# Kernel optimization log

Hardware: AMD Instinct MI355X
Metric: run time of the kernel (lower is better)

## Reference

```python
import jax, jax.numpy as jnp
import numpy as np

N = 4096      # nodes in the propagation tree batch
D = 5000      # input (BoW/TF-IDF) feature dim
H = 512       # hidden_dim
C = 4         # n_class
L = 8         # number of tree levels


def setup_inputs() -> dict:
    key = jax.random.key(0)
    ks = jax.random.split(key, 12)
    init = lambda k, shape, fan: (jax.random.normal(k, shape, jnp.float32)
                                  / np.float32(np.sqrt(fan)))
    x = jax.random.normal(ks[0], (N, D), jnp.float32)
    adj = jax.random.uniform(ks[1], (N, N), jnp.float32)
    level = jax.random.randint(ks[2], (N,), 0, L, jnp.int32)
    return {
        "x": x,
        "adj": adj,
        "level": level,
        "E_w": init(ks[3], (H, D), D),
        "Wr": init(ks[4], (H, H), H),
        "Wz": init(ks[5], (H, H), H),
        "Ur": init(ks[6], (H, H), H),
        "Uz": init(ks[7], (H, H), H),
        "Wh": init(ks[8], (H, H), H),
        "Uh": init(ks[9], (H, H), H),
        "dec_w": init(ks[10], (C, H), H),
        "dec_b": jnp.zeros((C,), jnp.float32),
        "n_levels": L,
    }


def reference(x, adj, level, E_w, Wr, Wz, Ur, Uz, Wh, Uh, dec_w, dec_b, n_levels):
    # x_hat = E(x): [N, H]
    x_hat = x @ E_w.T
    # precompute gate input contributions from x_hat (constant across levels)
    xr = x_hat @ Wr.T
    xz = x_hat @ Wz.T
    xh = x_hat @ Wh.T
    h = jnp.zeros_like(x_hat)  # [N, H]
    # bottom-up over tree levels (deepest level first, root = level 0)
    for j in reversed(range(n_levels)):
        mask = (level == j).astype(x_hat.dtype)[:, None]  # [N, 1]
        # level_adj.mm(h): aggregate children states into current-level rows
        hs = mask * (adj @ h)                              # [N, H]
        r = jax.nn.sigmoid(xr + hs @ Ur.T)
        z = jax.nn.sigmoid(xz + hs @ Uz.T)
        hj_hat = jnp.tanh(xh + (hs * r) @ Uh.T)
        hj = (1.0 - z) * hs + z * hj_hat
        h = h + mask * hj
    # decoder(h): [N, C]
    return h @ dec_w.T + dec_b
```

## Files before the change

kernel.cpp:

```cpp
#include <hip/hip_runtime.h>
#include <math.h>


#define NNODE 4096
#define DD 5000
#define DP 5024
#define HH 512
#define HHHH 262144
#define LL 8
#define PMAX 640
#define AKS 8
#define AKC 512
#define STR 40
#define NHt 2097152
#define XCH 1696
#define EWP (HH * DP)

typedef __attribute__((ext_vector_type(8))) short short8v;
typedef __attribute__((ext_vector_type(4))) float float4v;

union fu { float f; unsigned u; };

__device__ __forceinline__ float sigf(float x) { return 1.0f / (1.0f + __expf(-x)); }
__device__ __forceinline__ float bf2f(ushort b) { fu v; v.u = ((unsigned)b) << 16; return v.f; }

__device__ __forceinline__ void splitpair(float a, float b, unsigned& hi,
                                          unsigned& mi, unsigned& lo) {
  const unsigned M = 0xFFFF0000u;
  fu A, B; A.f = a; B.f = b;
  hi = (A.u >> 16) | (B.u & M);
  fu Ah, Bh; Ah.u = A.u & M; Bh.u = B.u & M;
  float ra = a - Ah.f, rb = b - Bh.f;
  fu A1, B1; A1.f = ra; B1.f = rb;
  mi = (A1.u >> 16) | (B1.u & M);
  fu A1h, B1h; A1h.u = A1.u & M; B1h.u = B1.u & M;
  float ra2 = ra - A1h.f, rb2 = rb - B1h.f;
  fu A2, B2; A2.f = ra2; B2.f = rb2;
  lo = (A2.u >> 16) | (B2.u & M);
}

__device__ __forceinline__ void split8(const float* v, uint4& h, uint4& m, uint4& l) {
  splitpair(v[0], v[1], h.x, m.x, l.x);
  splitpair(v[2], v[3], h.y, m.y, l.y);
  splitpair(v[4], v[5], h.z, m.z, l.z);
  splitpair(v[6], v[7], h.w, m.w, l.w);
}

__device__ __forceinline__ void split1(float x, ushort& h, ushort& m, ushort& l) {
  const unsigned M = 0xFFFF0000u;
  fu a; a.f = x; h = (ushort)(a.u >> 16);
  fu ah; ah.u = a.u & M; float r = x - ah.f;
  fu b; b.f = r; m = (ushort)(b.u >> 16);
  fu bh; bh.u = b.u & M; float r2 = r - bh.f;
  fu c; c.f = r2; l = (ushort)(c.u >> 16);
}

template <int NB, int AROWS, int BROWS>
__device__ __forceinline__ void mfma6(const ushort* As, const ushort* Bs,
                                      int wm, int wn, int lr, int lg8,
                                      float4v (*acc)[NB]) {
  short8v a[2][3];
#pragma unroll
  for (int im = 0; im < 2; ++im)
#pragma unroll
    for (int p = 0; p < 3; ++p)
      a[im][p] = *reinterpret_cast<const short8v*>(
          &As[(p * AROWS + wm + 16 * im + lr) * STR + lg8]);
  short8v b[NB][3];
#pragma unroll
  for (int in = 0; in < NB; ++in)
#pragma unroll
    for (int p = 0; p < 3; ++p)
      b[in][p] = *reinterpret_cast<const short8v*>(
          &Bs[(p * BROWS + wn + 16 * in + lr) * STR + lg8]);
#pragma unroll
  for (int im = 0; im < 2; ++im)
#pragma unroll
    for (int in = 0; in < NB; ++in) {
      float4v c = acc[im][in];
      c = __builtin_amdgcn_mfma_f32_16x16x32_bf16(a[im][0], b[in][0], c, 0, 0, 0);
      c = __builtin_amdgcn_mfma_f32_16x16x32_bf16(a[im][0], b[in][1], c, 0, 0, 0);
      c = __builtin_amdgcn_mfma_f32_16x16x32_bf16(a[im][1], b[in][0], c, 0, 0, 0);
      c = __builtin_amdgcn_mfma_f32_16x16x32_bf16(a[im][0], b[in][2], c, 0, 0, 0);
      c = __builtin_amdgcn_mfma_f32_16x16x32_bf16(a[im][2], b[in][0], c, 0, 0, 0);
      c = __builtin_amdgcn_mfma_f32_16x16x32_bf16(a[im][1], b[in][1], c, 0, 0, 0);
      acc[im][in] = c;
    }
}

__global__ __launch_bounds__(256) void build_lists(const int* __restrict__ level,
                                                   int* __restrict__ counts,
                                                   int* __restrict__ rows, int N) {
  int i = blockIdx.x * blockDim.x + threadIdx.x;
  if (i < N) {
    int j = level[i];
    int p = atomicAdd(&counts[j], 1);
    rows[(size_t)j * N + p] = i;
  }
}

__global__ __launch_bounds__(256) void cast_all(
    const float* __restrict__ Ur, const float* __restrict__ Uz,
    const float* __restrict__ Uh, const float* __restrict__ Wr,
    const float* __restrict__ Wz, const float* __restrict__ Wh,
    ushort* __restrict__ urz3, ushort* __restrict__ uh3,
    ushort* __restrict__ w3s) {
  const int y = blockIdx.y;
  const float* src = (y == 0) ? Ur : (y == 1) ? Uz : (y == 2) ? Uh
                   : (y == 3) ? Wr : (y == 4) ? Wz : Wh;
  ushort* dst; size_t ps, off;
  if (y <= 1)      { dst = urz3; ps = 2 * (size_t)HHHH; off = (size_t)y * HHHH; }
  else if (y == 2) { dst = uh3;  ps = HHHH; off = 0; }
  else             { dst = w3s + (size_t)(y - 3) * 3 * HHHH; ps = HHHH; off = 0; }
  int i = (blockIdx.x * 256 + threadIdx.x) * 8;
  float4 t0 = *reinterpret_cast<const float4*>(src + i);
  float4 t1 = *reinterpret_cast<const float4*>(src + i + 4);
  float v[8] = {t0.x, t0.y, t0.z, t0.w, t1.x, t1.y, t1.z, t1.w};
  uint4 h, m, l;
  split8(v, h, m, l);
  *reinterpret_cast<uint4*>(dst + off + i) = h;
  *reinterpret_cast<uint4*>(dst + ps + off + i) = m;
  *reinterpret_cast<uint4*>(dst + 2 * ps + off + i) = l;
}

__global__ __launch_bounds__(256) void cast_ew(const float* __restrict__ Ew,
                                               ushort* __restrict__ ew3) {
  int idx = (blockIdx.x * 256 + threadIdx.x) * 8;
  int row = idx / DP, col = idx % DP;
  float v[8];
  if (col + 8 <= DD) {
    float4 t0 = *reinterpret_cast<const float4*>(Ew + (size_t)row * DD + col);
    float4 t1 = *reinterpret_cast<const float4*>(Ew + (size_t)row * DD + col + 4);
    v[0]=t0.x; v[1]=t0.y; v[2]=t0.z; v[3]=t0.w;
    v[4]=t1.x; v[5]=t1.y; v[6]=t1.z; v[7]=t1.w;
  } else {
#pragma unroll
    for (int i = 0; i < 8; ++i)
      v[i] = (col + i < DD) ? Ew[(size_t)row * DD + col + i] : 0.0f;
  }
  uint4 h, m, l;
  split8(v, h, m, l);
  *reinterpret_cast<uint4*>(ew3 + idx) = h;
  *reinterpret_cast<uint4*>(ew3 + EWP + idx) = m;
  *reinterpret_cast<uint4*>(ew3 + 2 * (size_t)EWP + idx) = l;
}

__global__ __launch_bounds__(256) void gemm_xhat_sk(const float* __restrict__ x,
                                                    const ushort* __restrict__ ew3,
                                                    float* __restrict__ xpart) {
  __shared__ ushort As[3 * 64 * STR];
  __shared__ ushort Bs[3 * 128 * STR];
  const int z = blockIdx.z;
  const int kb = z * XCH;
  const int kePad = min(kb + XCH, DP);
  const int keReal = min(kePad, DD);
  const int tid = threadIdx.x;
  const int bm = blockIdx.x * 64, bn = blockIdx.y * 128;
  const int wid = tid >> 6, lane = tid & 63;
  const int lr = lane & 15, lg = lane >> 4, lg8 = lg * 8;
  const int wm = (wid >> 1) * 32, wn = (wid & 1) * 64;
  const int ar = tid >> 2, akq = (tid & 3) * 8;
  const int br = tid >> 1, bkq = (tid & 1) * 16;
  const float* ap = x + (size_t)(bm + ar) * DD + kb + akq;
  const ushort* bph = ew3 + (size_t)(bn + br) * DP + kb + bkq;
  float4v acc[2][4];
#pragma unroll
  for (int i = 0; i < 2; ++i)
#pragma unroll
    for (int j = 0; j < 4; ++j) acc[i][j] = (float4v){0.f, 0.f, 0.f, 0.f};
  uint4 ah, am, al;
  short8v b0[3], b1[3];
  auto loadA = [&](int k0) {
    float v[8];
    if (k0 + 32 <= keReal) {
      float4 t0 = *reinterpret_cast<const float4*>(ap);
      float4 t1 = *reinterpret_cast<const float4*>(ap + 4);
      v[0]=t0.x; v[1]=t0.y; v[2]=t0.z; v[3]=t0.w;
      v[4]=t1.x; v[5]=t1.y; v[6]=t1.z; v[7]=t1.w;
    } else {
#pragma unroll
      for (int i = 0; i < 8; ++i) v[i] = (k0 + akq + i < keReal) ? ap[i] : 0.0f;
    }
    split8(v, ah, am, al);
    ap += 32;
  };
  auto loadB = [&]() {
#pragma unroll
    for (int p = 0; p < 3; ++p) {
      b0[p] = *reinterpret_cast<const short8v*>(bph + (size_t)p * EWP);
      b1[p] = *reinterpret_cast<const short8v*>(bph + (size_t)p * EWP + 8);
    }
    bph += 32;
  };
  loadA(kb); loadB();
  for (int k0 = kb; k0 < kePad; k0 += 32) {
    __syncthreads();
    *reinterpret_cast<uint4*>(&As[(0 * 64 + ar) * STR + akq]) = ah;
    *reinterpret_cast<uint4*>(&As[(1 * 64 + ar) * STR + akq]) = am;
    *reinterpret_cast<uint4*>(&As[(2 * 64 + ar) * STR + akq]) = al;
#pragma unroll
    for (int p = 0; p < 3; ++p) {
      *reinterpret_cast<short8v*>(&Bs[(p * 128 + br) * STR + bkq]) = b0[p];
      *reinterpret_cast<short8v*>(&Bs[(p * 128 + br) * STR + bkq + 8]) = b1[p];
    }
    __syncthreads();
    if (k0 + 32 < kePad) { loadA(k0 + 32); loadB(); }
    mfma6<4, 64, 128>(As, Bs, wm, wn, lr, lg8, acc);
  }
  float* C = xpart + (size_t)z * NHt;
#pragma unroll
  for (int im = 0; im < 2; ++im)
#pragma unroll
    for (int in = 0; in < 4; ++in)
#pragma unroll
      for (int r = 0; r < 4; ++r)
        C[(size_t)(bm + wm + im * 16 + lg * 4 + r) * HH + bn + wn + in * 16 + lr] =
            acc[im][in][r];
}

__global__ __launch_bounds__(256) void combine3(const float* __restrict__ p,
                                                ushort* __restrict__ xh3) {
  int i = (blockIdx.x * 256 + threadIdx.x) * 8;
  float v[8];
#pragma unroll
  for (int e = 0; e < 8; e += 4) {
    float4 a = *reinterpret_cast<const float4*>(p + i + e);
    float4 b = *reinterpret_cast<const float4*>(p + NHt + i + e);
    float4 c = *reinterpret_cast<const float4*>(p + 2 * (size_t)NHt + i + e);
    v[e + 0] = a.x + b.x + c.x; v[e + 1] = a.y + b.y + c.y;
    v[e + 2] = a.z + b.z + c.z; v[e + 3] = a.w + b.w + c.w;
  }
  uint4 h, m, l;
  split8(v, h, m, l);
  *reinterpret_cast<uint4*>(xh3 + i) = h;
  *reinterpret_cast<uint4*>(xh3 + NHt + i) = m;
  *reinterpret_cast<uint4*>(xh3 + 2 * (size_t)NHt + i) = l;
}

__global__ __launch_bounds__(256) void gemm_w36(const ushort* __restrict__ xh3,
                                                const ushort* __restrict__ w3s,
                                                float* __restrict__ xrzh) {
  const int z = blockIdx.z;
  const ushort* B = w3s + (size_t)z * 3 * HHHH;
  float* C = xrzh + (size_t)z * NHt;
  __shared__ ushort As[3 * 64 * STR];
  __shared__ ushort Bs[3 * 128 * STR];
  const int tid = threadIdx.x;
  const int bm = blockIdx.x * 64, bn = blockIdx.y * 128;
  const int wid = tid >> 6, lane = tid & 63;
  const int lr = lane & 15, lg = lane >> 4, lg8 = lg * 8;
  const int wm = (wid >> 1) * 32, wn = (wid & 1) * 64;
  const int ar = tid >> 2, akq = (tid & 3) * 8;
  const int br = tid >> 1, bkq = (tid & 1) * 16;
  const ushort* aph = xh3 + (size_t)(bm + ar) * HH + akq;
  const ushort* bph = B + (size_t)(bn + br) * HH + bkq;
  float4v acc[2][4];
#pragma unroll
  for (int i = 0; i < 2; ++i)
#pragma unroll
    for (int j = 0; j < 4; ++j) acc[i][j] = (float4v){0.f, 0.f, 0.f, 0.f};
  short8v a3[3], b0[3], b1[3];
  auto loadAll = [&]() {
#pragma unroll
    for (int p = 0; p < 3; ++p) {
      a3[p] = *reinterpret_cast<const short8v*>(aph + (size_t)p * NHt);
      b0[p] = *reinterpret_cast<const short8v*>(bph + (size_t)p * HHHH);
      b1[p] = *reinterpret_cast<const short8v*>(bph + (size_t)p * HHHH + 8);
    }
    aph += 32; bph += 32;
  };
  loadAll();
  for (int k0 = 0; k0 < HH; k0 += 32) {
    __syncthreads();
#pragma unroll
    for (int p = 0; p < 3; ++p) {
      *reinterpret_cast<short8v*>(&As[(p * 64 + ar) * STR + akq]) = a3[p];
      *reinterpret_cast<short8v*>(&Bs[(p * 128 + br) * STR + bkq]) = b0[p];
      *reinterpret_cast<short8v*>(&Bs[(p * 128 + br) * STR + bkq + 8]) = b1[p];
    }
    __syncthreads();
    if (k0 + 32 < HH) loadAll();
    mfma6<4, 64, 128>(As, Bs, wm, wn, lr, lg8, acc);
  }
#pragma unroll
  for (int im = 0; im < 2; ++im)
#pragma unroll
    for (int in = 0; in < 4; ++in)
#pragma unroll
      for (int r = 0; r < 4; ++r)
        C[(size_t)(bm + wm + im * 16 + lg * 4 + r) * HH + bn + wn + in * 16 + lr] =
            acc[im][in][r];
}

__global__ __launch_bounds__(256) void agg6(const float* __restrict__ adj,
                                            const ushort* __restrict__ hT3,
                                            const int* __restrict__ rows,
                                            const int* __restrict__ counts,
                                            int lvl, float* __restrict__ part) {
  const int cnt = min(counts[lvl], PMAX);
  const int bm = blockIdx.x * 32;
  if (bm >= cnt) return;
  const int* rl = rows + (size_t)lvl * NNODE;
  const int kb = blockIdx.z * AKC;
  const int bn = blockIdx.y * 128;
  __shared__ ushort As[3 * 32 * STR];
  __shared__ ushort Bs[3 * 128 * STR];
  const int tid = threadIdx.x;
  const int wid = tid >> 6, lane = tid & 63;
  const int lr = lane & 15, lg = lane >> 4, lg8 = lg * 8;
  const int wn = wid * 32;
  const int ar = (tid & 127) >> 2, akq = (tid & 3) * 8;
  const int br = tid >> 1, bkq = (tid & 1) * 16;
  int p0 = bm + ar;
  if (p0 >= cnt) p0 = cnt - 1;
  const float* ap = adj + (size_t)rl[p0] * NNODE + kb + akq;
  const ushort* bph = hT3 + (size_t)(bn + br) * NNODE + kb + bkq;
  float4v acc[2][2];
#pragma unroll
  for (int i = 0; i < 2; ++i)
#pragma unroll
    for (int j = 0; j < 2; ++j) acc[i][j] = (float4v){0.f, 0.f, 0.f, 0.f};
  uint4 ah, am, al;
  short8v b0[3], b1[3];
  auto loadA = [&]() {
    float4 t0 = *reinterpret_cast<const float4*>(ap);
    float4 t1 = *reinterpret_cast<const float4*>(ap + 4);
    float v[8] = {t0.x, t0.y, t0.z, t0.w, t1.x, t1.y, t1.z, t1.w};
    split8(v, ah, am, al);
    ap += 32;
  };
  auto loadB = [&]() {
#pragma unroll
    for (int p = 0; p < 3; ++p) {
      b0[p] = *reinterpret_cast<const short8v*>(bph + (size_t)p * NHt);
      b1[p] = *reinterpret_cast<const short8v*>(bph + (size_t)p * NHt + 8);
    }
    bph += 32;
  };
  if (tid < 128) loadA();
  loadB();
  for (int k0 = 0; k0 < AKC; k0 += 32) {
    __syncthreads();
    if (tid < 128) {
      *reinterpret_cast<uint4*>(&As[(0 * 32 + ar) * STR + akq]) = ah;
      *reinterpret_cast<uint4*>(&As[(1 * 32 + ar) * STR + akq]) = am;
      *reinterpret_cast<uint4*>(&As[(2 * 32 + ar) * STR + akq]) = al;
    }
#pragma unroll
    for (int p = 0; p < 3; ++p) {
      *reinterpret_cast<short8v*>(&Bs[(p * 128 + br) * STR + bkq]) = b0[p];
      *reinterpret_cast<short8v*>(&Bs[(p * 128 + br) * STR + bkq + 8]) = b1[p];
    }
    __syncthreads();
    if (k0 + 32 < AKC) {
      if (tid < 128) loadA();
      loadB();
    }
    mfma6<2, 32, 128>(As, Bs, 0, wn, lr, lg8, acc);
  }
  float* cp = part + (size_t)blockIdx.z * PMAX * HH;
#pragma unroll
  for (int im = 0; im < 2; ++im)
#pragma unroll
    for (int in = 0; in < 2; ++in)
#pragma unroll
      for (int r = 0; r < 4; ++r) {
        int p = bm + 16 * im + lg * 4 + r;
        if (p < cnt)
          cp[(size_t)p * HH + bn + wn + in * 16 + lr] = acc[im][in][r];
      }
}

__global__ __launch_bounds__(256) void agg_reduce6(const float* __restrict__ part,
                                                   float* __restrict__ hsf,
                                                   ushort* __restrict__ hs3) {
  int id = blockIdx.x * 256 + threadIdx.x;
  const int zs = PMAX * HH / 4;
  const float4* q = reinterpret_cast<const float4*>(part) + id;
  float4 s = q[0];
#pragma unroll
  for (int z = 1; z < AKS; ++z) {
    float4 t = q[(size_t)z * zs];
    s.x += t.x; s.y += t.y; s.z += t.z; s.w += t.w;
  }
  reinterpret_cast<float4*>(hsf)[id] = s;
  unsigned h0, m0, l0, h1, m1, l1;
  splitpair(s.x, s.y, h0, m0, l0);
  splitpair(s.z, s.w, h1, m1, l1);
  *reinterpret_cast<uint2*>(hs3 + (size_t)id * 4) = make_uint2(h0, h1);
  *reinterpret_cast<uint2*>(hs3 + PMAX * HH + (size_t)id * 4) = make_uint2(m0, m1);
  *reinterpret_cast<uint2*>(hs3 + 2 * PMAX * HH + (size_t)id * 4) = make_uint2(l0, l1);
}

__global__ __launch_bounds__(256) void gates_rz6(
    const ushort* __restrict__ hs3, const ushort* __restrict__ urz3,
    const float* __restrict__ xr, const float* __restrict__ xz,
    const float* __restrict__ hsf, const int* __restrict__ rows,
    const int* __restrict__ counts, int lvl, ushort* __restrict__ tb3,
    float* __restrict__ zb) {
  const int cnt = min(counts[lvl], PMAX);
  const int bm = blockIdx.x * 32;
  if (bm >= cnt) return;
  const int* rl = rows + (size_t)lvl * NNODE;
  const int bn = blockIdx.y * 64;
  __shared__ ushort As[3 * 32 * STR];
  __shared__ ushort Bs[3 * 64 * STR];
  const int tid = threadIdx.x;
  const int wid = tid >> 6, lane = tid & 63;
  const int lr = lane & 15, lg = lane >> 4, lg8 = lg * 8;
  const int wn = wid * 16;
  const int ar = (tid & 127) >> 2, akq = (tid & 3) * 8;
  const int br = tid >> 2, bkq = (tid & 3) * 8;
  const ushort* aph = hs3 + (size_t)(bm + ar) * HH + akq;
  const ushort* bph = urz3 + (size_t)(bn + br) * HH + bkq;
  float4v acc[2][1];
  acc[0][0] = (float4v){0.f, 0.f, 0.f, 0.f};
  acc[1][0] = (float4v){0.f, 0.f, 0.f, 0.f};
  short8v a3[3], b3[3];
  auto loadA = [&]() {
#pragma unroll
    for (int p = 0; p < 3; ++p)
      a3[p] = *reinterpret_cast<const short8v*>(aph + (size_t)p * PMAX * HH);
    aph += 32;
  };
  auto loadB = [&]() {
#pragma unroll
    for (int p = 0; p < 3; ++p)
      b3[p] = *reinterpret_cast<const short8v*>(bph + (size_t)p * 2 * HHHH);
    bph += 32;
  };
  if (tid < 128) loadA();
  loadB();
  for (int k0 = 0; k0 < HH; k0 += 32) {
    __syncthreads();
    if (tid < 128) {
#pragma unroll
      for (int p = 0; p < 3; ++p)
        *reinterpret_cast<short8v*>(&As[(p * 32 + ar) * STR + akq]) = a3[p];
    }
#pragma unroll
    for (int p = 0; p < 3; ++p)
      *reinterpret_cast<short8v*>(&Bs[(p * 64 + br) * STR + bkq]) = b3[p];
    __syncthreads();
    if (k0 + 32 < HH) {
      if (tid < 128) loadA();
      loadB();
    }
    mfma6<1, 32, 64>(As, Bs, 0, wn, lr, lg8, acc);
  }
  ushort* th = tb3;
  ushort* tm = tb3 + PMAX * HH;
  ushort* tl = tb3 + 2 * PMAX * HH;
#pragma unroll
  for (int im = 0; im < 2; ++im)
#pragma unroll
    for (int r = 0; r < 4; ++r) {
      int p = bm + 16 * im + lg * 4 + r;
      if (p < cnt) {
        int col = bn + wn + lr;
        int g = rl[p];
        if (col < HH) {
          float rr = sigf(xr[(size_t)g * HH + col] + acc[im][0][r]);
          float t = hsf[(size_t)p * HH + col] * rr;
          ushort h, m, l;
          split1(t, h, m, l);
          size_t idx = (size_t)p * HH + col;
          th[idx] = h; tm[idx] = m; tl[idx] = l;
        } else {
          int c = col - HH;
          zb[(size_t)p * HH + c] = sigf(xz[(size_t)g * HH + c] + acc[im][0][r]);
        }
      }
    }
}

__global__ __launch_bounds__(256) void gates_h6(
    const ushort* __restrict__ tb3, const ushort* __restrict__ uh3,
    const float* __restrict__ xh, const float* __restrict__ hsf,
    const float* __restrict__ zb, const int* __restrict__ rows,
    const int* __restrict__ counts, int lvl, ushort* __restrict__ hT3) {
  const int cnt = min(counts[lvl], PMAX);
  const int bm = blockIdx.x * 32;
  if (bm >= cnt) return;
  const int* rl = rows + (size_t)lvl * NNODE;
  const int bn = blockIdx.y * 64;
  __shared__ ushort As[3 * 32 * STR];
  __shared__ ushort Bs[3 * 64 * STR];
  const int tid = threadIdx.x;
  const int wid = tid >> 6, lane = tid & 63;
  const int lr = lane & 15, lg = lane >> 4, lg8 = lg * 8;
  const int wn = wid * 16;
  const int ar = (tid & 127) >> 2, akq = (tid & 3) * 8;
  const int br = tid >> 2, bkq = (tid & 3) * 8;
  const ushort* aph = tb3 + (size_t)(bm + ar) * HH + akq;
  const ushort* bph = uh3 + (size_t)(bn + br) * HH + bkq;
  float4v acc[2][1];
  acc[0][0] = (float4v){0.f, 0.f, 0.f, 0.f};
  acc[1][0] = (float4v){0.f, 0.f, 0.f, 0.f};
  short8v a3[3], b3[3];
  auto loadA = [&]() {
#pragma unroll
    for (int p = 0; p < 3; ++p)
      a3[p] = *reinterpret_cast<const short8v*>(aph + (size_t)p * PMAX * HH);
    aph += 32;
  };
  auto loadB = [&]() {
#pragma unroll
    for (int p = 0; p < 3; ++p)
      b3[p] = *reinterpret_cast<const short8v*>(bph + (size_t)p * HHHH);
    bph += 32;
  };
  if (tid < 128) loadA();
  loadB();
  for (int k0 = 0; k0 < HH; k0 += 32) {
    __syncthreads();
    if (tid < 128) {
#pragma unroll
      for (int p = 0; p < 3; ++p)
        *reinterpret_cast<short8v*>(&As[(p * 32 + ar) * STR + akq]) = a3[p];
    }
#pragma unroll
    for (int p = 0; p < 3; ++p)
      *reinterpret_cast<short8v*>(&Bs[(p * 64 + br) * STR + bkq]) = b3[p];
    __syncthreads();
    if (k0 + 32 < HH) {
      if (tid < 128) loadA();
      loadB();
    }
    mfma6<1, 32, 64>(As, Bs, 0, wn, lr, lg8, acc);
  }
  ushort* hp = hT3;
  ushort* mp = hT3 + NHt;
  ushort* lp = hT3 + 2 * (size_t)NHt;
#pragma unroll
  for (int im = 0; im < 2; ++im)
#pragma unroll
    for (int r = 0; r < 4; ++r) {
      int p = bm + 16 * im + lg * 4 + r;
      if (p < cnt) {
        int col = bn + wn + lr;
        int g = rl[p];
        size_t idx = (size_t)p * HH + col;
        float hh = tanhf(xh[(size_t)g * HH + col] + acc[im][0][r]);
        float zz = zb[idx];
        float hv = (1.0f - zz) * hsf[idx] + zz * hh;
        ushort h, m, l;
        split1(hv, h, m, l);
        size_t tix = (size_t)col * NNODE + g;
        hp[tix] = h; mp[tix] = m; lp[tix] = l;
      }
    }
}

__global__ __launch_bounds__(256) void lvl7_init(const float* __restrict__ xz,
                                                 const float* __restrict__ xh,
                                                 const int* __restrict__ rows,
                                                 const int* __restrict__ counts,
                                                 ushort* __restrict__ hT3) {
  const int cnt = min(counts[LL - 1], PMAX);
  int idx = blockIdx.x * 256 + threadIdx.x;
  int p = idx >> 6;
  int c0 = (idx & 63) * 8;
  if (p >= cnt) return;
  int g = rows[(size_t)(LL - 1) * NNODE + p];
  float4 z0 = *reinterpret_cast<const float4*>(xz + (size_t)g * HH + c0);
  float4 z1 = *reinterpret_cast<const float4*>(xz + (size_t)g * HH + c0 + 4);
  float4 h0 = *reinterpret_cast<const float4*>(xh + (size_t)g * HH + c0);
  float4 h1 = *reinterpret_cast<const float4*>(xh + (size_t)g * HH + c0 + 4);
  float zv[8] = {z0.x, z0.y, z0.z, z0.w, z1.x, z1.y, z1.z, z1.w};
  float hv[8] = {h0.x, h0.y, h0.z, h0.w, h1.x, h1.y, h1.z, h1.w};
#pragma unroll
  for (int i = 0; i < 8; ++i) {
    float val = sigf(zv[i]) * tanhf(hv[i]);
    ushort h, m, l;
    split1(val, h, m, l);
    size_t tix = (size_t)(c0 + i) * NNODE + g;
    hT3[tix] = h;
    hT3[NHt + tix] = m;
    hT3[2 * (size_t)NHt + tix] = l;
  }
}

__global__ __launch_bounds__(256) void decoder6(const ushort* __restrict__ hT3,
                                                const float* __restrict__ w,
                                                const float* __restrict__ b,
                                                float* __restrict__ out) {
  int g = blockIdx.x * 256 + threadIdx.x;
  float a0 = 0.f, a1 = 0.f, a2 = 0.f, a3 = 0.f;
#pragma unroll 4
  for (int c = 0; c < HH; ++c) {
    size_t idx = (size_t)c * NNODE + g;
    float hv = bf2f(hT3[idx]) + bf2f(hT3[NHt + idx]) +
               bf2f(hT3[2 * (size_t)NHt + idx]);
    a0 = fmaf(hv, w[c], a0);
    a1 = fmaf(hv, w[HH + c], a1);
    a2 = fmaf(hv, w[2 * HH + c], a2);
    a3 = fmaf(hv, w[3 * HH + c], a3);
  }
  float4 o = make_float4(a0 + b[0], a1 + b[1], a2 + b[2], a3 + b[3]);
  *reinterpret_cast<float4*>(out + (size_t)g * 4) = o;
}

extern "C" void kernel_launch(void* const* d_in, const int* in_sizes, int n_in,
                              void* d_out, int out_size, void* d_ws,
                              size_t ws_size, hipStream_t stream) {
  const float* x   = (const float*)d_in[0];
  const float* adj = (const float*)d_in[1];
  const int* level = (const int*)d_in[2];
  const float* E_w = (const float*)d_in[3];
  const float* Wr  = (const float*)d_in[4];
  const float* Wz  = (const float*)d_in[5];
  const float* Ur  = (const float*)d_in[6];
  const float* Uz  = (const float*)d_in[7];
  const float* Wh  = (const float*)d_in[8];
  const float* Uh  = (const float*)d_in[9];
  const float* dw  = (const float*)d_in[10];
  const float* db  = (const float*)d_in[11];

  char* wp = (char*)d_ws;
  ushort* urz3 = (ushort*)wp; wp += (size_t)3 * 2 * HHHH * 2;
  ushort* uh3  = (ushort*)wp; wp += (size_t)3 * HHHH * 2;
  ushort* w3s  = (ushort*)wp; wp += (size_t)3 * 3 * HHHH * 2;
  ushort* hT3  = (ushort*)wp; wp += (size_t)3 * NHt * 2;
  float*  xrzh = (float*)wp;  wp += (size_t)3 * NHt * 4;
  char* region = wp;
  ushort* ew3  = (ushort*)region;
  float*  part = (float*)region;
  ushort* tb3  = (ushort*)(region + (size_t)AKS * PMAX * HH * 4);
  float*  zb   = (float*)((char*)tb3 + (size_t)3 * PMAX * HH * 2);
  float*  hsf  = (float*)((char*)zb + (size_t)PMAX * HH * 4);
  ushort* hs3  = (ushort*)((char*)hsf + (size_t)PMAX * HH * 4);
  size_t regionBytes = (size_t)3 * EWP * 2;
  size_t lvlBytes = (size_t)AKS * PMAX * HH * 4 + (size_t)3 * PMAX * HH * 2 +
                    (size_t)PMAX * HH * 4 + (size_t)PMAX * HH * 4 +
                    (size_t)3 * PMAX * HH * 2;
  if (lvlBytes > regionBytes) regionBytes = lvlBytes;
  wp = region + regionBytes;
  int* counts = (int*)wp; wp += 64;
  int* rowsl  = (int*)wp; wp += (size_t)LL * NNODE * 4;
  if (ws_size < (size_t)(wp - (char*)d_ws)) return;

  ushort* xh3 = hT3;
  float* xpart = xrzh;

  hipMemsetAsync(counts, 0, 64, stream);
  build_lists<<<(NNODE + 255) / 256, 256, 0, stream>>>(level, counts, rowsl, NNODE);
  cast_all<<<dim3(HHHH / 8 / 256, 6), 256, 0, stream>>>(Ur, Uz, Uh, Wr, Wz, Wh,
                                                        urz3, uh3, w3s);
  cast_ew<<<dim3(HH * DP / 8 / 256), 256, 0, stream>>>(E_w, ew3);
  gemm_xhat_sk<<<dim3(NNODE / 64, HH / 128, 3), 256, 0, stream>>>(x, ew3, xpart);
  combine3<<<NHt / 8 / 256, 256, 0, stream>>>(xpart, xh3);
  gemm_w36<<<dim3(NNODE / 64, HH / 128, 3), 256, 0, stream>>>(xh3, w3s, xrzh);

  const float* xr  = xrzh;
  const float* xzp = xrzh + (size_t)NHt;
  const float* xhp = xrzh + (size_t)2 * NHt;

  hipMemsetAsync(hT3, 0, (size_t)3 * NHt * 2, stream);
  lvl7_init<<<PMAX * HH / 8 / 256, 256, 0, stream>>>(xzp, xhp, rowsl, counts, hT3);

  for (int j = LL - 2; j >= 0; --j) {
    agg6<<<dim3(PMAX / 32, HH / 128, AKS), 256, 0, stream>>>(adj, hT3, rowsl,
                                                             counts, j, part);
    agg_reduce6<<<PMAX * HH / 4 / 256, 256, 0, stream>>>(part, hsf, hs3);
    gates_rz6<<<dim3(PMAX / 32, 2 * HH / 64), 256, 0, stream>>>(
        hs3, urz3, xr, xzp, hsf, rowsl, counts, j, tb3, zb);
    gates_h6<<<dim3(PMAX / 32, HH / 64), 256, 0, stream>>>(
        tb3, uh3, xhp, hsf, zb, rowsl, counts, j, hT3);
  }
  decoder6<<<dim3(NNODE / 256), 256, 0, stream>>>(hT3, dw, db, (float*)d_out);
}
```

Baseline: 821.4 us.

## Store hidden states in level order and aggregate only over deeper-level nodes

Builds a level-ordered permutation of nodes, deepest levels first, and stores the transposed hidden states in that order. The aggregation GEMM for each level now runs its K loop only over nodes from deeper levels, since all other hidden rows are still zero. The split-K chunk size is computed dynamically. This removes roughly half of the multiply-accumulate work and the hidden-state reads in the adj @ h step. In exchange, adjacency values are now read as scattered per-element gathers through the permutation rather than contiguous vector loads, and the decoder and gate kernels must remap indices.

Measured after the change: 839.6 us. +2.2%, slower.

```diff
diff --git a/kernel.cpp b/kernel.cpp
--- a/kernel.cpp
+++ b/kernel.cpp
@@ -10,7 +10,6 @@
 #define LL 8
 #define PMAX 640
 #define AKS 8
-#define AKC 512
 #define STR 40
 #define NHt 2097152
 #define XCH 1696
@@ -23,6 +22,13 @@
 
 __device__ __forceinline__ float sigf(float x) { return 1.0f / (1.0f + __expf(-x)); }
 __device__ __forceinline__ float bf2f(ushort b) { fu v; v.u = ((unsigned)b) << 16; return v.f; }
+
+__device__ __forceinline__ int prefix_above(const int* __restrict__ counts,
+                                            int lvl) {
+  int s = 0;
+  for (int i = lvl + 1; i < LL; ++i) s += min(counts[i], PMAX);
+  return s;
+}
 
 __device__ __forceinline__ void splitpair(float a, float b, unsigned& hi,
                                           unsigned& mi, unsigned& lo) {
@@ -97,6 +103,16 @@
     int p = atomicAdd(&counts[j], 1);
     rows[(size_t)j * N + p] = i;
   }
+}
+
+__global__ __launch_bounds__(256) void build_order(const int* __restrict__ counts,
+                                                   const int* __restrict__ rows,
+                                                   int* __restrict__ actord) {
+  const int j = blockIdx.y;
+  const int cnt = min(counts[j], PMAX);
+  const int off = prefix_above(counts, j);
+  int p = blockIdx.x * 256 + threadIdx.x;
+  if (p < cnt) actord[off + p] = rows[(size_t)j * NNODE + p];
 }
 
 __global__ __launch_bounds__(256) void cast_all(
@@ -296,12 +312,16 @@
                                             const ushort* __restrict__ hT3,
                                             const int* __restrict__ rows,
                                             const int* __restrict__ counts,
+                                            const int* __restrict__ actord,
                                             int lvl, float* __restrict__ part) {
   const int cnt = min(counts[lvl], PMAX);
   const int bm = blockIdx.x * 32;
   if (bm >= cnt) return;
+  const int K = prefix_above(counts, lvl);
+  const int chunk = ((K + AKS * 32 - 1) / (AKS * 32)) * 32;
+  const int kb = blockIdx.z * chunk;
+  const int ke = min(kb + chunk, K);
   const int* rl = rows + (size_t)lvl * NNODE;
-  const int kb = blockIdx.z * AKC;
   const int bn = blockIdx.y * 128;
   __shared__ ushort As[3 * 32 * STR];
   __shared__ ushort Bs[3 * 128 * STR];
@@ -313,7 +333,8 @@
   const int br = tid >> 1, bkq = (tid & 1) * 16;
   int p0 = bm + ar;
   if (p0 >= cnt) p0 = cnt - 1;
-  const float* ap = adj + (size_t)rl[p0] * NNODE + kb + akq;
+  const float* adjrow = adj + (size_t)rl[p0] * NNODE;
+  const int* aop = actord + kb + akq;
   const ushort* bph = hT3 + (size_t)(bn + br) * NNODE + kb + bkq;
   float4v acc[2][2];
 #pragma unroll
@@ -323,11 +344,12 @@
   uint4 ah, am, al;
   short8v b0[3], b1[3];
   auto loadA = [&]() {
-    float4 t0 = *reinterpret_cast<const float4*>(ap);
-    float4 t1 = *reinterpret_cast<const float4*>(ap + 4);
-    float v[8] = {t0.x, t0.y, t0.z, t0.w, t1.x, t1.y, t1.z, t1.w};
+    int4 i0 = *reinterpret_cast<const int4*>(aop);
+    int4 i1 = *reinterpret_cast<const int4*>(aop + 4);
+    float v[8] = {adjrow[i0.x], adjrow[i0.y], adjrow[i0.z], adjrow[i0.w],
+                  adjrow[i1.x], adjrow[i1.y], adjrow[i1.z], adjrow[i1.w]};
     split8(v, ah, am, al);
-    ap += 32;
+    aop += 32;
   };
   auto loadB = [&]() {
 #pragma unroll
@@ -337,9 +359,11 @@
     }
     bph += 32;
   };
-  if (tid < 128) loadA();
-  loadB();
-  for (int k0 = 0; k0 < AKC; k0 += 32) {
+  if (kb < ke) {
+    if (tid < 128) loadA();
+    loadB();
+  }
+  for (int k0 = kb; k0 < ke; k0 += 32) {
     __syncthreads();
     if (tid < 128) {
       *reinterpret_cast<uint4*>(&As[(0 * 32 + ar) * STR + akq]) = ah;
@@ -352,7 +376,7 @@
       *reinterpret_cast<short8v*>(&Bs[(p * 128 + br) * STR + bkq + 8]) = b1[p];
     }
     __syncthreads();
-    if (k0 + 32 < AKC) {
+    if (k0 + 32 < ke) {
       if (tid < 128) loadA();
       loadB();
     }
@@ -482,6 +506,7 @@
   const int cnt = min(counts[lvl], PMAX);
   const int bm = blockIdx.x * 32;
   if (bm >= cnt) return;
+  const int poff = prefix_above(counts, lvl);
   const int* rl = rows + (size_t)lvl * NNODE;
   const int bn = blockIdx.y * 64;
   __shared__ ushort As[3 * 32 * STR];
@@ -546,7 +571,7 @@
         float hv = (1.0f - zz) * hsf[idx] + zz * hh;
         ushort h, m, l;
         split1(hv, h, m, l);
-        size_t tix = (size_t)col * NNODE + g;
+        size_t tix = (size_t)col * NNODE + (poff + p);
         hp[tix] = h; mp[tix] = m; lp[tix] = l;
       }
     }
@@ -574,7 +599,7 @@
     float val = sigf(zv[i]) * tanhf(hv[i]);
     ushort h, m, l;
     split1(val, h, m, l);
-    size_t tix = (size_t)(c0 + i) * NNODE + g;
+    size_t tix = (size_t)(c0 + i) * NNODE + p;
     hT3[tix] = h;
     hT3[NHt + tix] = m;
     hT3[2 * (size_t)NHt + tix] = l;
@@ -582,14 +607,16 @@
 }
 
 __global__ __launch_bounds__(256) void decoder6(const ushort* __restrict__ hT3,
+                                                const int* __restrict__ actord,
                                                 const float* __restrict__ w,
                                                 const float* __restrict__ b,
                                                 float* __restrict__ out) {
-  int g = blockIdx.x * 256 + threadIdx.x;
+  int p = blockIdx.x * 256 + threadIdx.x;
+  int g = actord[p];
   float a0 = 0.f, a1 = 0.f, a2 = 0.f, a3 = 0.f;
 #pragma unroll 4
   for (int c = 0; c < HH; ++c) {
-    size_t idx = (size_t)c * NNODE + g;
+    size_t idx = (size_t)c * NNODE + p;
     float hv = bf2f(hT3[idx]) + bf2f(hT3[NHt + idx]) +
                bf2f(hT3[2 * (size_t)NHt + idx]);
     a0 = fmaf(hv, w[c], a0);
@@ -638,6 +665,7 @@
   wp = region + regionBytes;
   int* counts = (int*)wp; wp += 64;
   int* rowsl  = (int*)wp; wp += (size_t)LL * NNODE * 4;
+  int* actord = (int*)wp; wp += (size_t)NNODE * 4;
   if (ws_size < (size_t)(wp - (char*)d_ws)) return;
 
   ushort* xh3 = hT3;
@@ -645,6 +673,8 @@
 
   hipMemsetAsync(counts, 0, 64, stream);
   build_lists<<<(NNODE + 255) / 256, 256, 0, stream>>>(level, counts, rowsl, NNODE);
+  build_order<<<dim3((PMAX + 255) / 256, LL), 256, 0, stream>>>(counts, rowsl,
+                                                                actord);
   cast_all<<<dim3(HHHH / 8 / 256, 6), 256, 0, stream>>>(Ur, Uz, Uh, Wr, Wz, Wh,
                                                         urz3, uh3, w3s);
   cast_ew<<<dim3(HH * DP / 8 / 256), 256, 0, stream>>>(E_w, ew3);
@@ -660,13 +690,14 @@
   lvl7_init<<<PMAX * HH / 8 / 256, 256, 0, stream>>>(xzp, xhp, rowsl, counts, hT3);
 
   for (int j = LL - 2; j >= 0; --j) {
-    agg6<<<dim3(PMAX / 32, HH / 128, AKS), 256, 0, stream>>>(adj, hT3, rowsl,
-                                                             counts, j, part);
+    agg6<<<dim3(PMAX / 32, HH / 128, AKS), 256, 0, stream>>>(
+        adj, hT3, rowsl, counts, actord, j, part);
     agg_reduce6<<<PMAX * HH / 4 / 256, 256, 0, stream>>>(part, hsf, hs3);
     gates_rz6<<<dim3(PMAX / 32, 2 * HH / 64), 256, 0, stream>>>(
         hs3, urz3, xr, xzp, hsf, rowsl, counts, j, tb3, zb);
     gates_h6<<<dim3(PMAX / 32, HH / 64), 256, 0, stream>>>(
         tb3, uh3, xhp, hsf, zb, rowsl, counts, j, hT3);
   }
-  decoder6<<<dim3(NNODE / 256), 256, 0, stream>>>(hT3, dw, db, (float*)d_out);
-}
+  decoder6<<<dim3(NNODE / 256), 256, 0, stream>>>(hT3, actord, dw, db,
+                                                  (float*)d_out);
+}
```
